# Kernel optimization log

Hardware: AMD Instinct MI355X
Metric: run time of the kernel (lower is better)

Reference implementation:

```python
import jax, jax.numpy as jnp
import numpy as np

KH, KW = 3, 3
STRIDE = (1, 1)
PAD = (1, 1)
DIL = (1, 1)
DG = 1  # num_deformable_groups


def _out_size(h, pad, dil, k, stride):
    return (h + 2 * pad - (dil * (k - 1) + 1)) // stride + 1


def setup_inputs() -> dict:
    key = jax.random.key(0)
    k1, k2, k3 = jax.random.split(key, 3)
    B, Cin, H, W = 8, 128, 64, 64
    Cout = 128
    Ho = _out_size(H, PAD[0], DIL[0], KH, STRIDE[0])
    Wo = _out_size(W, PAD[1], DIL[1], KW, STRIDE[1])
    x = jax.random.normal(k1, (B, Cin, H, W), jnp.float32)
    offset = jax.random.normal(k2, (B, 2 * DG * KH * KW, Ho, Wo), jnp.float32)
    n = Cin * KH * KW
    stdv = 1.0 / np.sqrt(n)
    weight = jax.random.uniform(k3, (Cout, Cin, KH, KW), jnp.float32, -stdv, stdv)
    return {"x": x, "offset": offset, "weight": weight}


def deform_conv2d(x, offset, weight):
    B, Cin, H, W = x.shape
    Cout, _, kh, kw = weight.shape
    K = kh * kw
    Ho = _out_size(H, PAD[0], DIL[0], kh, STRIDE[0])
    Wo = _out_size(W, PAD[1], DIL[1], kw, STRIDE[1])
    G = DG
    Cg = Cin // G

    # base sampling grid per kernel tap: [kh,kw,Ho,Wo]
    by = (jnp.arange(kh) * DIL[0])[:, None, None, None] + (jnp.arange(Ho) * STRIDE[0] - PAD[0])[None, None, :, None]
    bx = (jnp.arange(kw) * DIL[1])[None, :, None, None] + (jnp.arange(Wo) * STRIDE[1] - PAD[1])[None, None, None, :]
    by = jnp.broadcast_to(by, (kh, kw, Ho, Wo)).reshape(K, Ho, Wo).astype(x.dtype)
    bx = jnp.broadcast_to(bx, (kh, kw, Ho, Wo)).reshape(K, Ho, Wo).astype(x.dtype)

    # offset layout: channel = g*2*K + 2*k + {0: dy, 1: dx}
    off = offset.reshape(B, G, K, 2, Ho, Wo)
    py = by[None, None] + off[:, :, :, 0]  # [B,G,K,Ho,Wo]
    px = bx[None, None] + off[:, :, :, 1]

    y0 = jnp.floor(py).astype(jnp.int32)
    x0 = jnp.floor(px).astype(jnp.int32)
    wy = (py - y0).reshape(B, G, 1, -1)  # fractional parts, [B,G,1,K*Ho*Wo]
    wx = (px - x0).reshape(B, G, 1, -1)

    xg = x.reshape(B, G, Cg, H * W)
    N = K * Ho * Wo

    def gather(yi, xi):
        valid = ((yi >= 0) & (yi < H) & (xi >= 0) & (xi < W)).reshape(B, G, 1, N)
        idx = (jnp.clip(yi, 0, H - 1) * W + jnp.clip(xi, 0, W - 1)).reshape(B, G, 1, N)
        v = jnp.take_along_axis(xg, jnp.broadcast_to(idx, (B, G, Cg, N)), axis=3)
        return v * valid.astype(x.dtype)

    v00 = gather(y0, x0)
    v01 = gather(y0, x0 + 1)
    v10 = gather(y0 + 1, x0)
    v11 = gather(y0 + 1, x0 + 1)

    cols = (v00 * (1 - wy) * (1 - wx) + v01 * (1 - wy) * wx
            + v10 * wy * (1 - wx) + v11 * wy * wx)
    cols = cols.reshape(B, G, Cg, K, Ho, Wo)  # deformable im2col columns

    wr = weight.reshape(Cout, G, Cg, K)
    return jnp.einsum('ogck,bgcknm->bonm', wr, cols)


def reference(x, offset, weight):
    return deform_conv2d(x, offset, weight)
```

## Files before the change

kernel.cpp:

```cpp
#include <hip/hip_runtime.h>
#include <hip/hip_fp16.h>

typedef __attribute__((ext_vector_type(4))) float f32x4;
typedef __attribute__((ext_vector_type(8))) _Float16 f16x8;
typedef __attribute__((ext_vector_type(4))) unsigned int u32x4;

__device__ __forceinline__ unsigned short f2h(float f) {
  __half h = __float2half_rn(f);
  unsigned short u;
  __builtin_memcpy(&u, &h, 2);
  return u;
}
__device__ __forceinline__ __half2 h2_of(unsigned int u) {
  __half2 h;
  __builtin_memcpy(&h, &u, 4);
  return h;
}
__device__ __forceinline__ unsigned int u_of(__half2 h) {
  unsigned int u;
  __builtin_memcpy(&u, &h, 4);
  return u;
}

__global__ __launch_bounds__(256) void prep_kernel(const float* __restrict__ w,
                                                   unsigned short* __restrict__ wf) {
  int tid = blockIdx.x * 256 + threadIdx.x;
  int l  = tid & 63;
  int mt = (tid >> 6) & 7;
  int ch = tid >> 9;
  int cc = ch / 9, tap = ch - cc * 9;
  int co = mt * 16 + (l & 15);
  int cb = cc * 32 + (l >> 4) * 8;
  unsigned int r[8];
#pragma unroll
  for (int j = 0; j < 8; ++j)
    r[j] = f2h(w[(co * 128 + cb + j) * 9 + tap]);
  u32x4 pk;
  pk.x = r[0] | (r[1] << 16);
  pk.y = r[2] | (r[3] << 16);
  pk.z = r[4] | (r[5] << 16);
  pk.w = r[6] | (r[7] << 16);
  *reinterpret_cast<u32x4*>(wf + (size_t)tid * 8) = pk;
}

__global__ __launch_bounds__(512, 1) void deform_kernel(const float* __restrict__ x,
                                                        const float* __restrict__ off,
                                                        const unsigned short* __restrict__ wf,
                                                        float* __restrict__ out) {
  __shared__ __align__(16) unsigned char sWin[8 * 17408];
  __shared__ int2  sPA[1152];
  __shared__ uint2 sWt[1152];

  const int tid = threadIdx.x;
  const int bid = blockIdx.x;
  const int b   = bid & 7;
  const int ho0 = (bid >> 3) * 2;
  const int r0  = min(max(ho0 - 3, 0), 56);

  {
    const float* xb = x + ((size_t)b << 19) + ((size_t)r0 << 6);
#pragma unroll
    for (int it = 0; it < 16; ++it) {
      int idx = it * 512 + tid;
      int p  = idx & 63;
      int r  = (idx >> 6) & 7;
      int cg = idx >> 9;
      const float* xp = xb + (((size_t)cg) << 15) + (r << 6) + p;
      unsigned int q[8];
#pragma unroll
      for (int j = 0; j < 8; ++j) q[j] = f2h(xp[(size_t)j << 12]);
      u32x4 pk;
      pk.x = q[0] | (q[1] << 16);
      pk.y = q[2] | (q[3] << 16);
      pk.z = q[4] | (q[5] << 16);
      pk.w = q[6] | (q[7] << 16);
      *reinterpret_cast<u32x4*>(&sWin[r * 17408 + p * 272 + cg * 16]) = pk;
    }
  }

  for (int r = tid; r < 1152; r += 512) {
    int row = (r >= 576) ? 1 : 0;
    int rr  = r - row * 576;
    int tap = rr >> 6, wo = rr & 63;
    int ho = ho0 + row;
    float dy = off[((b * 18 + 2 * tap)     * 64 + ho) * 64 + wo];
    float dx = off[((b * 18 + 2 * tap + 1) * 64 + ho) * 64 + wo];
    float py = (float)(ho + (tap / 3) - 1) + dy;
    float px = (float)(wo + (tap % 3) - 1) + dx;
    float fy = floorf(py), fx = floorf(px);
    int y0 = (int)fy, x0 = (int)fx;
    float wy = py - fy, wx = px - fx;
    float wt = (y0 >= 0 && y0 < 64) ? (1.f - wy) : 0.f;
    float wb = (y0 + 1 >= 0 && y0 + 1 < 64) ? wy : 0.f;
    int y0c = min(max(y0, 0), 63), y1c = min(max(y0 + 1, 0), 63);
    int bx; float wl, wr;
    if (x0 >= 0 && x0 <= 62)      { bx = x0; wl = 1.f - wx; wr = wx;       }
    else if (x0 == -1)            { bx = 0;  wl = wx;       wr = 0.f;      }
    else if (x0 == 63)            { bx = 62; wl = 0.f;      wr = 1.f - wx; }
    else                          { bx = 0;  wl = 0.f;      wr = 0.f;      }
    int aX = y0c * 64 + bx, aY = y1c * 64 + bx;
    int twr = y0c - r0, bwr = y1c - r0;
    int tin = ((unsigned)twr < 8u) ? 1 : 0;
    int bin = ((unsigned)bwr < 8u) ? 1 : 0;
    int laT0 = (tin ? twr : 0) * 17408 + bx * 272;
    int laB0 = (bin ? bwr : 0) * 17408 + bx * 272;
    int2 pw;
    pw.x = laT0 | (aX << 18) | (tin ? 0 : (int)0x80000000);
    pw.y = laB0 | (aY << 18) | (bin ? 0 : (int)0x80000000);
    sPA[r] = pw;
    __half2 tp = __floats2half2_rn(wt * wl, wt * wr);
    __half2 bp = __floats2half2_rn(wb * wl, wb * wr);
    uint2 ww;
    ww.x = u_of(tp);
    ww.y = u_of(bp);
    sWt[r] = ww;
  }
  __syncthreads();

  const int l   = tid & 63;
  const int w   = tid >> 6;
  const int ks  = w & 3;
  const int row = w >> 2;
  const int ln  = l & 15;
  const int kg  = l >> 4;
  const int koff = ks * 64 + kg * 16;
  const int ho  = ho0 + row;

  const float* xfb = x + ((size_t)b << 19) + (((size_t)(ks * 32 + kg * 8)) << 12);
  const unsigned short* wfb = wf + (size_t)l * 8;

  f32x4 acc[4][8] = {};

  for (int tap = 0; tap < 9; ++tap) {
    const int ch = ks * 9 + tap;

    f16x8 A[8];
    const unsigned short* wp = wfb + (size_t)(ch * 8) * 512;
#pragma unroll
    for (int mt = 0; mt < 8; ++mt)
      A[mt] = *reinterpret_cast<const f16x8*>(wp + (size_t)mt * 512);

    u32x4 T0[4], T1[4], B0[4], B1[4];
    uint2 wws[4];
#pragma unroll
    for (int pg = 0; pg < 4; ++pg) {
      const int e = row * 576 + tap * 64 + pg * 16 + ln;
      const int2 pa = sPA[e];
      wws[pg] = sWt[e];

      const int laT = (pa.x & 0x3FFFF) + koff;
      __builtin_memcpy(&T0[pg], &sWin[laT],       16);
      __builtin_memcpy(&T1[pg], &sWin[laT + 272], 16);
      const int laB = (pa.y & 0x3FFFF) + koff;
      __builtin_memcpy(&B0[pg], &sWin[laB],       16);
      __builtin_memcpy(&B1[pg], &sWin[laB + 272], 16);

      if (pa.x < 0) {
        const int aX = (pa.x >> 18) & 4095;
        const float* p0 = xfb + aX;
        u32x4 q0, q1;
#pragma unroll
        for (int d = 0; d < 4; ++d) {
          unsigned int a0 = f2h(p0[(size_t)(2 * d)     << 12]);
          unsigned int a1 = f2h(p0[(size_t)(2 * d + 1) << 12]);
          q0[d] = a0 | (a1 << 16);
          unsigned int c0 = f2h(p0[((size_t)(2 * d)     << 12) + 1]);
          unsigned int c1 = f2h(p0[((size_t)(2 * d + 1) << 12) + 1]);
          q1[d] = c0 | (c1 << 16);
        }
        T0[pg] = q0;
        T1[pg] = q1;
      }
      if (pa.y < 0) {
        const int aY = (pa.y >> 18) & 4095;
        const float* p1 = xfb + aY;
        u32x4 q0, q1;
#pragma unroll
        for (int d = 0; d < 4; ++d) {
          unsigned int a0 = f2h(p1[(size_t)(2 * d)     << 12]);
          unsigned int a1 = f2h(p1[(size_t)(2 * d + 1) << 12]);
          q0[d] = a0 | (a1 << 16);
          unsigned int c0 = f2h(p1[((size_t)(2 * d)     << 12) + 1]);
          unsigned int c1 = f2h(p1[((size_t)(2 * d + 1) << 12) + 1]);
          q1[d] = c0 | (c1 << 16);
        }
        B0[pg] = q0;
        B1[pg] = q1;
      }
    }

#pragma unroll
    for (int pg = 0; pg < 4; ++pg) {
      const uint2 ww = wws[pg];
      const __half2 wtl = __half2half2(__low2half(h2_of(ww.x)));
      const __half2 wtr = __half2half2(__high2half(h2_of(ww.x)));
      const __half2 wbl = __half2half2(__low2half(h2_of(ww.y)));
      const __half2 wbr = __half2half2(__high2half(h2_of(ww.y)));
      u32x4 pk;
#pragma unroll
      for (int d = 0; d < 4; ++d) {
        __half2 s = __hmul2(wtl, h2_of(T0[pg][d]));
        s = __hfma2(wtr, h2_of(T1[pg][d]), s);
        s = __hfma2(wbl, h2_of(B0[pg][d]), s);
        s = __hfma2(wbr, h2_of(B1[pg][d]), s);
        pk[d] = u_of(s);
      }
      f16x8 bfrag;
      __builtin_memcpy(&bfrag, &pk, 16);

#pragma unroll
      for (int mt = 0; mt < 8; ++mt)
        acc[pg][mt] = __builtin_amdgcn_mfma_f32_16x16x32_f16(A[mt], bfrag,
                                                             acc[pg][mt], 0, 0, 0);
    }
  }

  float* sF = reinterpret_cast<float*>(sWin);
#define WR_LDS(BASE)                                                           \
  { _Pragma("unroll") for (int pg = 0; pg < 4; ++pg)                           \
    _Pragma("unroll") for (int mt = 0; mt < 8; ++mt)                           \
      *reinterpret_cast<f32x4*>(&sF[(BASE) + row * 8448 + (pg * 16 + ln) * 132 + mt * 16 + kg * 4]) = acc[pg][mt]; }
#define RD_LDS(BASE)                                                           \
  { _Pragma("unroll") for (int pg = 0; pg < 4; ++pg)                           \
    _Pragma("unroll") for (int mt = 0; mt < 8; ++mt) {                         \
      f32x4 v = *reinterpret_cast<const f32x4*>(&sF[(BASE) + row * 8448 + (pg * 16 + ln) * 132 + mt * 16 + kg * 4]); \
      acc[pg][mt] += v; } }

  __syncthreads();
  if (ks == 1) WR_LDS(17408)
  if (ks == 3) WR_LDS(0)
  __syncthreads();
  if (ks == 0) RD_LDS(17408)
  if (ks == 2) RD_LDS(0)
  __syncthreads();
  if (ks == 2) WR_LDS(17408)
  __syncthreads();
  if (ks == 0) RD_LDS(17408)
#undef WR_LDS
#undef RD_LDS

  {
    const int b2 = row * 8704;
    if (ks == 0) {
#pragma unroll
      for (int pg = 0; pg < 4; ++pg)
#pragma unroll
        for (int mt = 0; mt < 8; ++mt)
#pragma unroll
          for (int rg = 0; rg < 4; ++rg)
            sF[b2 + (mt * 16 + kg * 4 + rg) * 68 + pg * 16 + ln] = acc[pg][mt][rg];
    }
    __syncthreads();
    if (ks == 0) {
      const int q4  = l & 15;
      const int ch2 = l >> 4;
      float* ob = out + (((size_t)b * 128) * 64 + ho) * 64 + q4 * 4;
#pragma unroll
      for (int i = 0; i < 32; ++i) {
        int co = ch2 * 32 + i;
        f32x4 v = *reinterpret_cast<const f32x4*>(&sF[b2 + co * 68 + q4 * 4]);
        *reinterpret_cast<f32x4*>(ob + (size_t)co * 4096) = v;
      }
    }
  }
}

extern "C" void kernel_launch(void* const* d_in, const int* in_sizes, int n_in,
                              void* d_out, int out_size, void* d_ws, size_t ws_size,
                              hipStream_t stream) {
  (void)in_sizes; (void)n_in; (void)out_size; (void)ws_size;
  const float* x   = (const float*)d_in[0];
  const float* off = (const float*)d_in[1];
  const float* w   = (const float*)d_in[2];
  float* out = (float*)d_out;
  unsigned short* wf = (unsigned short*)d_ws;

  prep_kernel<<<72, 256, 0, stream>>>(w, wf);
  deform_kernel<<<256, 512, 0, stream>>>(x, off, wf, out);
}
```

Before: 97.72 us.

## Merge sample tables and software-pipeline LDS gathers with MFMA in tap loop

Combines the per-sample address and bilinear-weight tables into a single int4 table so one LDS read fetches both. Prefetches the next tap's table entries during the current tap, and reorders the four pixel groups so LDS gathers for later groups are issued while earlier groups are interpolated and fed to MFMA, using a 3-slot register ring instead of 4. The aim is to hide LDS latency behind MFMA work and to cut the number of table loads. The cost is higher register pressure from the prefetched table entries, in a kernel already launched at 512 threads with a large accumulator array.

```diff
diff --git a/kernel.cpp b/kernel.cpp
--- a/kernel.cpp
+++ b/kernel.cpp
@@ -48,8 +48,7 @@
                                                         const unsigned short* __restrict__ wf,
                                                         float* __restrict__ out) {
   __shared__ __align__(16) unsigned char sWin[8 * 17408];
-  __shared__ int2  sPA[1152];
-  __shared__ uint2 sWt[1152];
+  __shared__ int4 sTab[1152];
 
   const int tid = threadIdx.x;
   const int bid = blockIdx.x;
@@ -104,16 +103,12 @@
     int bin = ((unsigned)bwr < 8u) ? 1 : 0;
     int laT0 = (tin ? twr : 0) * 17408 + bx * 272;
     int laB0 = (bin ? bwr : 0) * 17408 + bx * 272;
-    int2 pw;
+    int4 pw;
     pw.x = laT0 | (aX << 18) | (tin ? 0 : (int)0x80000000);
     pw.y = laB0 | (aY << 18) | (bin ? 0 : (int)0x80000000);
-    sPA[r] = pw;
-    __half2 tp = __floats2half2_rn(wt * wl, wt * wr);
-    __half2 bp = __floats2half2_rn(wb * wl, wb * wr);
-    uint2 ww;
-    ww.x = u_of(tp);
-    ww.y = u_of(bp);
-    sWt[r] = ww;
+    pw.z = (int)u_of(__floats2half2_rn(wt * wl, wt * wr));
+    pw.w = (int)u_of(__floats2half2_rn(wb * wl, wb * wr));
+    sTab[r] = pw;
   }
   __syncthreads();
 
@@ -125,95 +120,102 @@
   const int kg  = l >> 4;
   const int koff = ks * 64 + kg * 16;
   const int ho  = ho0 + row;
+  const int tbase = row * 576 + ln;
 
   const float* xfb = x + ((size_t)b << 19) + (((size_t)(ks * 32 + kg * 8)) << 12);
   const unsigned short* wfb = wf + (size_t)l * 8;
 
   f32x4 acc[4][8] = {};
 
+  int4 tbc[4];
+#pragma unroll
+  for (int pg = 0; pg < 4; ++pg) tbc[pg] = sTab[tbase + pg * 16];
+
+#define ISSUE(S, PG) {                                                         \
+    const int4 tb = tbc[PG];                                                   \
+    const int laT = (tb.x & 0x3FFFF) + koff;                                   \
+    __builtin_memcpy(&T0[S], &sWin[laT],       16);                            \
+    __builtin_memcpy(&T1[S], &sWin[laT + 272], 16);                            \
+    const int laB = (tb.y & 0x3FFFF) + koff;                                   \
+    __builtin_memcpy(&B0[S], &sWin[laB],       16);                            \
+    __builtin_memcpy(&B1[S], &sWin[laB + 272], 16);                            \
+    if (tb.x < 0) {    \
+      const float* p0 = xfb + ((tb.x >> 18) & 4095);                           \
+      u32x4 q0, q1;                                                            \
+      _Pragma("unroll") for (int d = 0; d < 4; ++d) {                          \
+        unsigned int a0 = f2h(p0[(size_t)(2 * d)     << 12]);                  \
+        unsigned int a1 = f2h(p0[(size_t)(2 * d + 1) << 12]);                  \
+        q0[d] = a0 | (a1 << 16);                                               \
+        unsigned int c0 = f2h(p0[((size_t)(2 * d)     << 12) + 1]);            \
+        unsigned int c1 = f2h(p0[((size_t)(2 * d + 1) << 12) + 1]);            \
+        q1[d] = c0 | (c1 << 16);                                               \
+      }                                                                        \
+      T0[S] = q0; T1[S] = q1;                                                  \
+    }                                                                          \
+    if (tb.y < 0) {                \
+      const float* p1 = xfb + ((tb.y >> 18) & 4095);                           \
+      u32x4 q0, q1;                                                            \
+      _Pragma("unroll") for (int d = 0; d < 4; ++d) {                          \
+        unsigned int a0 = f2h(p1[(size_t)(2 * d)     << 12]);                  \
+        unsigned int a1 = f2h(p1[(size_t)(2 * d + 1) << 12]);                  \
+        q0[d] = a0 | (a1 << 16);                                               \
+        unsigned int c0 = f2h(p1[((size_t)(2 * d)     << 12) + 1]);            \
+        unsigned int c1 = f2h(p1[((size_t)(2 * d + 1) << 12) + 1]);            \
+        q1[d] = c0 | (c1 << 16);                                               \
+      }                                                                        \
+      B0[S] = q0; B1[S] = q1;                                                  \
+    }                                                                          \
+  }
+
+#define INTERP(S, PG) {                                                        \
+    const __half2 wtl = __half2half2(__low2half(h2_of((unsigned)tbc[PG].z)));  \
+    const __half2 wtr = __half2half2(__high2half(h2_of((unsigned)tbc[PG].z))); \
+    const __half2 wbl = __half2half2(__low2half(h2_of((unsigned)tbc[PG].w)));  \
+    const __half2 wbr = __half2half2(__high2half(h2_of((unsigned)tbc[PG].w))); \
+    u32x4 pk;                                                                  \
+    _Pragma("unroll") for (int d = 0; d < 4; ++d) {                            \
+      __half2 s = __hmul2(wtl, h2_of(T0[S][d]));                               \
+      s = __hfma2(wtr, h2_of(T1[S][d]), s);                                    \
+      s = __hfma2(wbl, h2_of(B0[S][d]), s);                                    \
+      s = __hfma2(wbr, h2_of(B1[S][d]), s);                                    \
+      pk[d] = u_of(s);                                                         \
+    }                                                                          \
+    f16x8 bfrag;                                                               \
+    __builtin_memcpy(&bfrag, &pk, 16);                                         \
+    _Pragma("unroll") for (int mt = 0; mt < 8; ++mt)                           \
+      acc[PG][mt] = __builtin_amdgcn_mfma_f32_16x16x32_f16(A[mt], bfrag,       \
+                                                           acc[PG][mt], 0, 0, 0); \
+  }
+
   for (int tap = 0; tap < 9; ++tap) {
-    const int ch = ks * 9 + tap;
+    int4 tbn[4];
+    if (tap < 8) {
+#pragma unroll
+      for (int pg = 0; pg < 4; ++pg)
+        tbn[pg] = sTab[tbase + (tap + 1) * 64 + pg * 16];
+    }
 
     f16x8 A[8];
-    const unsigned short* wp = wfb + (size_t)(ch * 8) * 512;
+    const unsigned short* wp = wfb + (size_t)((ks * 9 + tap) * 8) * 512;
 #pragma unroll
     for (int mt = 0; mt < 8; ++mt)
       A[mt] = *reinterpret_cast<const f16x8*>(wp + (size_t)mt * 512);
 
-    u32x4 T0[4], T1[4], B0[4], B1[4];
-    uint2 wws[4];
-#pragma unroll
-    for (int pg = 0; pg < 4; ++pg) {
-      const int e = row * 576 + tap * 64 + pg * 16 + ln;
-      const int2 pa = sPA[e];
-      wws[pg] = sWt[e];
-
-      const int laT = (pa.x & 0x3FFFF) + koff;
-      __builtin_memcpy(&T0[pg], &sWin[laT],       16);
-      __builtin_memcpy(&T1[pg], &sWin[laT + 272], 16);
-      const int laB = (pa.y & 0x3FFFF) + koff;
-      __builtin_memcpy(&B0[pg], &sWin[laB],       16);
-      __builtin_memcpy(&B1[pg], &sWin[laB + 272], 16);
-
-      if (pa.x < 0) {
-        const int aX = (pa.x >> 18) & 4095;
-        const float* p0 = xfb + aX;
-        u32x4 q0, q1;
-#pragma unroll
-        for (int d = 0; d < 4; ++d) {
-          unsigned int a0 = f2h(p0[(size_t)(2 * d)     << 12]);
-          unsigned int a1 = f2h(p0[(size_t)(2 * d + 1) << 12]);
-          q0[d] = a0 | (a1 << 16);
-          unsigned int c0 = f2h(p0[((size_t)(2 * d)     << 12) + 1]);
-          unsigned int c1 = f2h(p0[((size_t)(2 * d + 1) << 12) + 1]);
-          q1[d] = c0 | (c1 << 16);
-        }
-        T0[pg] = q0;
-        T1[pg] = q1;
-      }
-      if (pa.y < 0) {
-        const int aY = (pa.y >> 18) & 4095;
-        const float* p1 = xfb + aY;
-        u32x4 q0, q1;
-#pragma unroll
-        for (int d = 0; d < 4; ++d) {
-          unsigned int a0 = f2h(p1[(size_t)(2 * d)     << 12]);
-          unsigned int a1 = f2h(p1[(size_t)(2 * d + 1) << 12]);
-          q0[d] = a0 | (a1 << 16);
-          unsigned int c0 = f2h(p1[((size_t)(2 * d)     << 12) + 1]);
-          unsigned int c1 = f2h(p1[((size_t)(2 * d + 1) << 12) + 1]);
-          q1[d] = c0 | (c1 << 16);
-        }
-        B0[pg] = q0;
-        B1[pg] = q1;
-      }
-    }
-
-#pragma unroll
-    for (int pg = 0; pg < 4; ++pg) {
-      const uint2 ww = wws[pg];
-      const __half2 wtl = __half2half2(__low2half(h2_of(ww.x)));
-      const __half2 wtr = __half2half2(__high2half(h2_of(ww.x)));
-      const __half2 wbl = __half2half2(__low2half(h2_of(ww.y)));
-      const __half2 wbr = __half2half2(__high2half(h2_of(ww.y)));
-      u32x4 pk;
-#pragma unroll
-      for (int d = 0; d < 4; ++d) {
-        __half2 s = __hmul2(wtl, h2_of(T0[pg][d]));
-        s = __hfma2(wtr, h2_of(T1[pg][d]), s);
-        s = __hfma2(wbl, h2_of(B0[pg][d]), s);
-        s = __hfma2(wbr, h2_of(B1[pg][d]), s);
-        pk[d] = u_of(s);
-      }
-      f16x8 bfrag;
-      __builtin_memcpy(&bfrag, &pk, 16);
-
-#pragma unroll
-      for (int mt = 0; mt < 8; ++mt)
-        acc[pg][mt] = __builtin_amdgcn_mfma_f32_16x16x32_f16(A[mt], bfrag,
-                                                             acc[pg][mt], 0, 0, 0);
-    }
-  }
+    u32x4 T0[3], T1[3], B0[3], B1[3];
+    ISSUE(0, 0)
+    ISSUE(1, 1)
+    ISSUE(2, 2)
+    INTERP(0, 0)
+    ISSUE(0, 3)
+    INTERP(1, 1)
+    INTERP(2, 2)
+    INTERP(0, 3)
+
+#pragma unroll
+    for (int pg = 0; pg < 4; ++pg) tbc[pg] = tbn[pg];
+  }
+#undef ISSUE
+#undef INTERP
 
   float* sF = reinterpret_cast<float*>(sWin);
 #define WR_LDS(BASE)                                                           \
```

New measurement: 96.58 us, median of 2. Within noise of the previous version (-1.2%).
